# Optimization experiments

Measured on AMD Instinct MI355X. Metric: run time of the kernel, lower is better.

The kernel has to match this reference:

```python
import jax, jax.numpy as jnp
import numpy as np

N_ATOMS = 20000
N_CG = 1000
N_EDGES = 200000
FEAT = 128
N_RBF = 20
N_CONV = 3
CUTOFF = 5.0
EPS = 1e-15


def swish(x):
    return x * jax.nn.sigmoid(x)


def preprocess_r(r):
    # r: (n, 3) -> dist (n,), unit (n, 3)
    d = jnp.sqrt((r * r + EPS).sum(-1))
    return d, r / d[:, None]


def dist_embed(d, W, b):
    # PainnRadialBasis (learnable_k=False) + Dense + cosine envelope
    k = jnp.arange(1, N_RBF + 1, dtype=d.dtype)
    rbf = jnp.sin(k[None, :] * jnp.pi * d[:, None] / CUTOFF) / d[:, None]
    env = 0.5 * (jnp.cos(jnp.pi * d / CUTOFF) + 1.0) * (d < CUTOFF).astype(d.dtype)
    return (rbf @ W + b) * env[:, None]


def scatter_mean(x, idx, n):
    s = jax.ops.segment_sum(x, idx, num_segments=n)
    cnt = jax.ops.segment_sum(jnp.ones(idx.shape[0], x.dtype), idx, num_segments=n)
    cnt = jnp.maximum(cnt, 1.0)
    return s / cnt.reshape((n,) + (1,) * (x.ndim - 1))


def cg_encoder(z, xyz, cg_xyz, mapping, nbr_list, embed,
               msg_W1, msg_b1, msg_W2, msg_b2, msg_distW, msg_distb,
               upd_U, upd_V, upd_W1, upd_b1, upd_W2, upd_b2,
               cg_W1, cg_b1, cg_W2, cg_b2, cg_distW, cg_distb):
    s = embed[z]                                     # (N, F)
    v = jnp.zeros((s.shape[0], FEAT, 3), s.dtype)    # (N, F, 3)
    src, dst = nbr_list[:, 0], nbr_list[:, 1]
    r_ij = xyz[dst] - xyz[src]
    r_iI = xyz - cg_xyz[mapping]
    d_ij, u_ij = preprocess_r(r_ij)
    d_iI, u_iI = preprocess_r(r_iI)

    S_I = None
    V_I = None
    for i in range(N_CONV):
        # ---- MessageBlock ----
        phi = swish(s @ msg_W1[i] + msg_b1[i]) @ msg_W2[i] + msg_b2[i]          # (N, 3F)
        w_s = dist_embed(d_ij, msg_distW[i], msg_distb[i])                      # (E, 3F)
        inv = (phi[dst] * w_s).reshape(-1, 3, FEAT)                             # (E, 3, F)
        dv_ij = inv[:, 2, :, None] * u_ij[:, None, :] + inv[:, 0, :, None] * v[dst]
        s = s + jax.ops.segment_sum(inv[:, 1, :], src, num_segments=N_ATOMS)
        v = v + jax.ops.segment_sum(dv_ij, src, num_segments=N_ATOMS)
        # ---- UpdateBlock ----
        u_v = jnp.einsum('nfd,fg->ngd', v, upd_U[i])
        v_v = jnp.einsum('nfd,fg->ngd', v, upd_V[i])
        v_v_norm = jnp.sqrt((v_v * v_v + EPS).sum(-1))                          # (N, F)
        stack = swish(jnp.concatenate([s, v_v_norm], -1) @ upd_W1[i] + upd_b1[i]) @ upd_W2[i] + upd_b2[i]
        a_vv = stack[:, :FEAT, None]
        a_sv = stack[:, FEAT:2 * FEAT]
        a_ss = stack[:, 2 * FEAT:]
        v = v + u_v * a_vv
        s = s + (u_v * v_v).sum(-1) * a_sv + a_ss
        # ---- init CG features after first conv ----
        if i == 0:
            S_I = scatter_mean(s, mapping, N_CG)
            V_I = jnp.zeros((N_CG, FEAT, 3), s.dtype)
        # ---- ContractiveMessageBlock ----
        phi_cg = swish(s @ cg_W1[i] + cg_b1[i]) @ cg_W2[i] + cg_b2[i]           # (N, 3F)
        w_cg = dist_embed(d_iI, cg_distW[i], cg_distb[i])
        inv_cg = (phi_cg * w_cg).reshape(-1, 3, FEAT)
        dv_iI = inv_cg[:, 2, :, None] * u_iI[:, None, :] + inv_cg[:, 0, :, None] * v
        S_I = S_I + scatter_mean(inv_cg[:, 1, :], mapping, N_CG)
        V_I = V_I + scatter_mean(dv_iI, mapping, N_CG)
    return S_I


def setup_inputs() -> dict:
    key = jax.random.key(0)
    ks = jax.random.split(key, 20)
    p = lambda i, shape: jax.random.normal(ks[i], shape, jnp.float32) * 0.05
    return {
        'z': jax.random.randint(ks[0], (N_ATOMS,), 1, 100),
        'xyz': jax.random.normal(ks[1], (N_ATOMS, 3), jnp.float32),
        'cg_xyz': jax.random.normal(ks[2], (N_CG, 3), jnp.float32),
        'mapping': jax.random.randint(ks[3], (N_ATOMS,), 0, N_CG),
        'nbr_list': jax.random.randint(ks[4], (N_EDGES, 2), 0, N_ATOMS),
        'embed': p(5, (100, FEAT)).at[0].set(0.0),  # padding_idx=0
        'msg_W1': p(6, (N_CONV, FEAT, FEAT)), 'msg_b1': jnp.zeros((N_CONV, FEAT)),
        'msg_W2': p(7, (N_CONV, FEAT, 3 * FEAT)), 'msg_b2': jnp.zeros((N_CONV, 3 * FEAT)),
        'msg_distW': p(8, (N_CONV, N_RBF, 3 * FEAT)), 'msg_distb': jnp.zeros((N_CONV, 3 * FEAT)),
        'upd_U': p(9, (N_CONV, FEAT, FEAT)), 'upd_V': p(10, (N_CONV, FEAT, FEAT)),
        'upd_W1': p(11, (N_CONV, 2 * FEAT, FEAT)), 'upd_b1': jnp.zeros((N_CONV, FEAT)),
        'upd_W2': p(12, (N_CONV, FEAT, 3 * FEAT)), 'upd_b2': jnp.zeros((N_CONV, 3 * FEAT)),
        'cg_W1': p(13, (N_CONV, FEAT, FEAT)), 'cg_b1': jnp.zeros((N_CONV, FEAT)),
        'cg_W2': p(14, (N_CONV, FEAT, 3 * FEAT)), 'cg_b2': jnp.zeros((N_CONV, 3 * FEAT)),
        'cg_distW': p(15, (N_CONV, N_RBF, 3 * FEAT)), 'cg_distb': jnp.zeros((N_CONV, 3 * FEAT)),
    }


def reference(z, xyz, cg_xyz, mapping, nbr_list, embed,
              msg_W1, msg_b1, msg_W2, msg_b2, msg_distW, msg_distb,
              upd_U, upd_V, upd_W1, upd_b1, upd_W2, upd_b2,
              cg_W1, cg_b1, cg_W2, cg_b2, cg_distW, cg_distb):
    return cg_encoder(z, xyz, cg_xyz, mapping, nbr_list, embed,
                      msg_W1, msg_b1, msg_W2, msg_b2, msg_distW, msg_distb,
                      upd_U, upd_V, upd_W1, upd_b1, upd_W2, upd_b2,
                      cg_W1, cg_b1, cg_W2, cg_b2, cg_distW, cg_distb)
```

## Files before the change

### kernel.cpp

```cpp
#include <hip/hip_runtime.h>
#include <math.h>

#define N_ATOMS 20000
#define N_CG    1000
#define N_EDGES 200000
#define FEAT    128
#define NRBF    20
#define NCONV   3
#define CUTOFF  5.0f
#define PLANE   (N_ATOMS * FEAT)
#define PI_F    3.14159265358979323846f
#define LDH     130

#define PACK_PER_CONV 212992

typedef __attribute__((ext_vector_type(8))) short bf16x8;
typedef __attribute__((ext_vector_type(4))) float f32x4;

__device__ __forceinline__ void split2(float x, ushort& h, ushort& l)
{
    unsigned u  = __float_as_uint(x);
    unsigned hb = (u + 0x7FFFu + ((u >> 16) & 1u)) & 0xFFFF0000u;
    float    hf = __uint_as_float(hb);
    float    lf = x - hf;
    unsigned ul = __float_as_uint(lf);
    h = (ushort)(hb >> 16);
    l = (ushort)((ul + 0x7FFFu + ((ul >> 16) & 1u)) >> 16);
}

__device__ __forceinline__ float reconP(unsigned u)
{
    return __uint_as_float(u & 0xFFFF0000u) + __uint_as_float(u << 16);
}

__device__ __forceinline__ unsigned packP(float x)
{
    ushort h, l;
    split2(x, h, l);
    return ((unsigned)h << 16) | l;
}

__device__ __forceinline__ void splitv8(const float* hv, bf16x8& ah, bf16x8& al)
{
#pragma unroll
    for (int j = 0; j < 8; ++j) {
        ushort h, l;
        split2(hv[j], h, l);
        ah[j] = (short)h; al[j] = (short)l;
    }
}

__device__ __forceinline__ void unpack8(const unsigned* __restrict__ p,
                                        bf16x8& ah, bf16x8& al)
{
#pragma unroll
    for (int j = 0; j < 8; ++j) {
        unsigned u = p[j];
        ah[j] = (short)(u >> 16);
        al[j] = (short)(u & 0xFFFFu);
    }
}

#define MFMA3(ACC, AH_, AL_, BH_, BL_)                                              \
    ACC = __builtin_amdgcn_mfma_f32_16x16x32_bf16(AH_, BH_, ACC, 0, 0, 0);          \
    ACC = __builtin_amdgcn_mfma_f32_16x16x32_bf16(AH_, BL_, ACC, 0, 0, 0);          \
    ACC = __builtin_amdgcn_mfma_f32_16x16x32_bf16(AL_, BH_, ACC, 0, 0, 0);

template<int K1, int N2>
__global__ __launch_bounds__(256)
void mlp_fused(const ushort* __restrict__ AH, const ushort* __restrict__ AL,
               const ushort* __restrict__ B1h, const ushort* __restrict__ B1l,
               const float* __restrict__ b1,
               const ushort* __restrict__ B2h, const ushort* __restrict__ B2l,
               const float* __restrict__ b2, int bcol0,
               float* __restrict__ C)
{
    __shared__ float Hs[32 * LDH];
    const int tid  = threadIdx.x;
    const int lane = tid & 63;
    const int w    = tid >> 6;
    const int wm   = w & 1, wn = w >> 1;
    const int m0   = blockIdx.x * 32;
    const int l15  = lane & 15;
    const int koff = (lane >> 4) * 8;
    const int rowb = wm * 16;
    const int q4   = (lane >> 4) * 4;

    f32x4 acc1[4];
#pragma unroll
    for (int j = 0; j < 4; ++j) acc1[j] = (f32x4){0.f, 0.f, 0.f, 0.f};
#pragma unroll
    for (int k0 = 0; k0 < K1; k0 += 32) {
        size_t aa = (size_t)(m0 + rowb + l15) * K1 + k0 + koff;
        bf16x8 ah = *reinterpret_cast<const bf16x8*>(AH + aa);
        bf16x8 al = *reinterpret_cast<const bf16x8*>(AL + aa);
#pragma unroll
        for (int nf = 0; nf < 4; ++nf) {
            size_t ba = (size_t)(wn * 64 + nf * 16 + l15) * K1 + k0 + koff;
            bf16x8 bh = *reinterpret_cast<const bf16x8*>(B1h + ba);
            bf16x8 bl = *reinterpret_cast<const bf16x8*>(B1l + ba);
            MFMA3(acc1[nf], ah, al, bh, bl);
        }
    }
#pragma unroll
    for (int nf = 0; nf < 4; ++nf) {
        int col = wn * 64 + nf * 16 + l15;
        float bv = b1[col];
#pragma unroll
        for (int r = 0; r < 4; ++r) {
            float x = acc1[nf][r] + bv;
            x = x / (1.f + __expf(-x));
            Hs[(rowb + q4 + r) * LDH + col] = x;
        }
    }
    __syncthreads();

    constexpr int NF2  = N2 / 32;
    constexpr int WCOL = N2 / 2;
    f32x4 acc2[NF2];
#pragma unroll
    for (int j = 0; j < NF2; ++j) acc2[j] = (f32x4){0.f, 0.f, 0.f, 0.f};
#pragma unroll
    for (int k0 = 0; k0 < 128; k0 += 32) {
        const float* hp = &Hs[(rowb + l15) * LDH + k0 + koff];
        float hv[8];
#pragma unroll
        for (int j = 0; j < 8; ++j) hv[j] = hp[j];
        bf16x8 ah, al;
        splitv8(hv, ah, al);
#pragma unroll
        for (int nf = 0; nf < NF2; ++nf) {
            size_t ba = (size_t)(wn * WCOL + nf * 16 + l15) * 128 + k0 + koff;
            bf16x8 bh = *reinterpret_cast<const bf16x8*>(B2h + ba);
            bf16x8 bl = *reinterpret_cast<const bf16x8*>(B2l + ba);
            MFMA3(acc2[nf], ah, al, bh, bl);
        }
    }
#pragma unroll
    for (int nf = 0; nf < NF2; ++nf) {
        int col = wn * WCOL + nf * 16 + l15;
        float bv = b2 ? b2[bcol0 + col] : 0.f;
#pragma unroll
        for (int r = 0; r < 4; ++r) {
            int row = m0 + rowb + q4 + r;
            C[(size_t)row * N2 + col] = acc2[nf][r] + bv;
        }
    }
}

__global__ __launch_bounds__(256)
void mlp_dual(const ushort* __restrict__ AH, const ushort* __restrict__ AL,
              const ushort* __restrict__ B1mh, const ushort* __restrict__ B1ml,
              const float* __restrict__ b1m,
              const ushort* __restrict__ B2mh, const ushort* __restrict__ B2ml,
              const float* __restrict__ b2m,
              const ushort* __restrict__ B1ch, const ushort* __restrict__ B1cl,
              const float* __restrict__ b1c,
              const ushort* __restrict__ B2ch, const ushort* __restrict__ B2cl,
              const float* __restrict__ b2c,
              float* __restrict__ Cm, float* __restrict__ Cc)
{
    __shared__ float Hm[32 * LDH];
    __shared__ float Hc[32 * LDH];
    const int tid  = threadIdx.x;
    const int lane = tid & 63;
    const int w    = tid >> 6;
    const int wm   = w & 1, wn = w >> 1;
    const int m0   = blockIdx.x * 32;
    const int l15  = lane & 15;
    const int koff = (lane >> 4) * 8;
    const int rowb = wm * 16;
    const int q4   = (lane >> 4) * 4;

    f32x4 am[4], ac[4];
#pragma unroll
    for (int j = 0; j < 4; ++j) {
        am[j] = (f32x4){0.f, 0.f, 0.f, 0.f};
        ac[j] = (f32x4){0.f, 0.f, 0.f, 0.f};
    }
#pragma unroll
    for (int k0 = 0; k0 < 128; k0 += 32) {
        size_t aa = (size_t)(m0 + rowb + l15) * 128 + k0 + koff;
        bf16x8 ah = *reinterpret_cast<const bf16x8*>(AH + aa);
        bf16x8 al = *reinterpret_cast<const bf16x8*>(AL + aa);
#pragma unroll
        for (int nf = 0; nf < 4; ++nf) {
            size_t ba = (size_t)(wn * 64 + nf * 16 + l15) * 128 + k0 + koff;
            bf16x8 bmh = *reinterpret_cast<const bf16x8*>(B1mh + ba);
            bf16x8 bml = *reinterpret_cast<const bf16x8*>(B1ml + ba);
            MFMA3(am[nf], ah, al, bmh, bml);
            bf16x8 bch = *reinterpret_cast<const bf16x8*>(B1ch + ba);
            bf16x8 bcl = *reinterpret_cast<const bf16x8*>(B1cl + ba);
            MFMA3(ac[nf], ah, al, bch, bcl);
        }
    }
#pragma unroll
    for (int nf = 0; nf < 4; ++nf) {
        int col = wn * 64 + nf * 16 + l15;
        float bvm = b1m[col];
        float bvc = b1c[col];
#pragma unroll
        for (int r = 0; r < 4; ++r) {
            int lr = rowb + q4 + r;
            float x = am[nf][r] + bvm;
            Hm[lr * LDH + col] = x / (1.f + __expf(-x));
            float y = ac[nf][r] + bvc;
            Hc[lr * LDH + col] = y / (1.f + __expf(-y));
        }
    }
    __syncthreads();

    f32x4 a2m[12], a2c[4];
#pragma unroll
    for (int j = 0; j < 12; ++j) a2m[j] = (f32x4){0.f, 0.f, 0.f, 0.f};
#pragma unroll
    for (int j = 0; j < 4; ++j)  a2c[j] = (f32x4){0.f, 0.f, 0.f, 0.f};
#pragma unroll
    for (int k0 = 0; k0 < 128; k0 += 32) {
        const float* hpm = &Hm[(rowb + l15) * LDH + k0 + koff];
        const float* hpc = &Hc[(rowb + l15) * LDH + k0 + koff];
        float hvm[8], hvc[8];
#pragma unroll
        for (int j = 0; j < 8; ++j) { hvm[j] = hpm[j]; hvc[j] = hpc[j]; }
        bf16x8 ahm, alm, ahc, alc;
        splitv8(hvm, ahm, alm);
        splitv8(hvc, ahc, alc);
#pragma unroll
        for (int nf = 0; nf < 12; ++nf) {
            size_t ba = (size_t)(wn * 192 + nf * 16 + l15) * 128 + k0 + koff;
            bf16x8 bh = *reinterpret_cast<const bf16x8*>(B2mh + ba);
            bf16x8 bl = *reinterpret_cast<const bf16x8*>(B2ml + ba);
            MFMA3(a2m[nf], ahm, alm, bh, bl);
        }
#pragma unroll
        for (int nf = 0; nf < 4; ++nf) {
            size_t ba = (size_t)(wn * 64 + nf * 16 + l15) * 128 + k0 + koff;
            bf16x8 bh = *reinterpret_cast<const bf16x8*>(B2ch + ba);
            bf16x8 bl = *reinterpret_cast<const bf16x8*>(B2cl + ba);
            MFMA3(a2c[nf], ahc, alc, bh, bl);
        }
    }
#pragma unroll
    for (int nf = 0; nf < 12; ++nf) {
        int col = wn * 192 + nf * 16 + l15;
        float bv = b2m[col];
#pragma unroll
        for (int r = 0; r < 4; ++r) {
            int row = m0 + rowb + q4 + r;
            Cm[(size_t)row * 384 + col] = a2m[nf][r] + bv;
        }
    }
#pragma unroll
    for (int nf = 0; nf < 4; ++nf) {
        int col = wn * 64 + nf * 16 + l15;
        float bv = b2c[128 + col];
#pragma unroll
        for (int r = 0; r < 4; ++r) {
            int row = m0 + rowb + q4 + r;
            Cc[(size_t)row * 128 + col] = a2c[nf][r] + bv;
        }
    }
}

__global__ __launch_bounds__(256)
void k_update_mega(unsigned* __restrict__ vP,
                   const ushort* __restrict__ catH, const ushort* __restrict__ catL,
                   const ushort* __restrict__ BVh, const ushort* __restrict__ BVl,
                   const ushort* __restrict__ W1h, const ushort* __restrict__ W1l,
                   const float*  __restrict__ b1,
                   const ushort* __restrict__ W2h, const ushort* __restrict__ W2l,
                   const float*  __restrict__ b2,
                   const ushort* __restrict__ BUh, const ushort* __restrict__ BUl,
                   float* __restrict__ s,
                   ushort* __restrict__ sH, ushort* __restrict__ sL)
{
    __shared__ float  Hs[32 * LDH];
    __shared__ ushort nH[32 * 128];
    __shared__ ushort nL[32 * 128];

    const int tid  = threadIdx.x;
    const int lane = tid & 63;
    const int w    = tid >> 6;
    const int wm   = w & 1, wn = w >> 1;
    const int m0   = blockIdx.x * 32;
    const int l15  = lane & 15;
    const int koff = (lane >> 4) * 8;
    const int rowb = wm * 16;
    const int q4   = (lane >> 4) * 4;

    f32x4 accV[3][4], accU[3][4];
#pragma unroll
    for (int d = 0; d < 3; ++d)
#pragma unroll
        for (int j = 0; j < 4; ++j) {
            accV[d][j] = (f32x4){0.f, 0.f, 0.f, 0.f};
            accU[d][j] = (f32x4){0.f, 0.f, 0.f, 0.f};
        }
    for (int k0 = 0; k0 < 128; k0 += 32) {
        bf16x8 ah[3], al[3];
#pragma unroll
        for (int d = 0; d < 3; ++d) {
            size_t aa = (size_t)d * PLANE + (size_t)(m0 + rowb + l15) * 128 + k0 + koff;
            unsigned u[8];
#pragma unroll
            for (int j = 0; j < 8; ++j) u[j] = vP[aa + j];
            unpack8(u, ah[d], al[d]);
        }
#pragma unroll
        for (int nf = 0; nf < 4; ++nf) {
            size_t ba = (size_t)(wn * 64 + nf * 16 + l15) * 128 + k0 + koff;
            bf16x8 bvh = *reinterpret_cast<const bf16x8*>(BVh + ba);
            bf16x8 bvl = *reinterpret_cast<const bf16x8*>(BVl + ba);
            bf16x8 buh = *reinterpret_cast<const bf16x8*>(BUh + ba);
            bf16x8 bul = *reinterpret_cast<const bf16x8*>(BUl + ba);
#pragma unroll
            for (int d = 0; d < 3; ++d) {
                MFMA3(accV[d][nf], ah[d], al[d], bvh, bvl);
            }
#pragma unroll
            for (int d = 0; d < 3; ++d) {
                MFMA3(accU[d][nf], ah[d], al[d], buh, bul);
            }
        }
    }
#pragma unroll
    for (int nf = 0; nf < 4; ++nf) {
        int col = wn * 64 + nf * 16 + l15;
#pragma unroll
        for (int r = 0; r < 4; ++r) {
            int lrow = rowb + q4 + r;
            float x = accV[0][nf][r], y = accV[1][nf][r], z = accV[2][nf][r];
            float nrm = sqrtf(x * x + y * y + z * z + 3e-15f);
            ushort h, l;
            split2(nrm, h, l);
            nH[lrow * 128 + col] = h;
            nL[lrow * 128 + col] = l;
        }
    }
    __syncthreads();

    f32x4 acc1[4];
#pragma unroll
    for (int j = 0; j < 4; ++j) acc1[j] = (f32x4){0.f, 0.f, 0.f, 0.f};
#pragma unroll 2
    for (int k0 = 0; k0 < 256; k0 += 32) {
        bf16x8 ah, al;
        if (k0 < 128) {
            size_t aa = (size_t)(m0 + rowb + l15) * 128 + k0 + koff;
            ah = *reinterpret_cast<const bf16x8*>(catH + aa);
            al = *reinterpret_cast<const bf16x8*>(catL + aa);
        } else {
            int la = (rowb + l15) * 128 + (k0 - 128) + koff;
            ah = *reinterpret_cast<const bf16x8*>(nH + la);
            al = *reinterpret_cast<const bf16x8*>(nL + la);
        }
#pragma unroll
        for (int nf = 0; nf < 4; ++nf) {
            size_t ba = (size_t)(wn * 64 + nf * 16 + l15) * 256 + k0 + koff;
            bf16x8 bh = *reinterpret_cast<const bf16x8*>(W1h + ba);
            bf16x8 bl = *reinterpret_cast<const bf16x8*>(W1l + ba);
            MFMA3(acc1[nf], ah, al, bh, bl);
        }
    }
#pragma unroll
    for (int nf = 0; nf < 4; ++nf) {
        int col = wn * 64 + nf * 16 + l15;
        float bv = b1[col];
#pragma unroll
        for (int r = 0; r < 4; ++r) {
            float x = acc1[nf][r] + bv;
            x = x / (1.f + __expf(-x));
            Hs[(rowb + q4 + r) * LDH + col] = x;
        }
    }
    __syncthreads();

    f32x4 acc2[12];
#pragma unroll
    for (int j = 0; j < 12; ++j) acc2[j] = (f32x4){0.f, 0.f, 0.f, 0.f};
    for (int k0 = 0; k0 < 128; k0 += 32) {
        const float* hp = &Hs[(rowb + l15) * LDH + k0 + koff];
        float hv[8];
#pragma unroll
        for (int j = 0; j < 8; ++j) hv[j] = hp[j];
        bf16x8 ah, al;
        splitv8(hv, ah, al);
#pragma unroll
        for (int g = 0; g < 3; ++g) {
#pragma unroll
            for (int j = 0; j < 4; ++j) {
                size_t ba = (size_t)(g * 128 + wn * 64 + j * 16 + l15) * 128 + k0 + koff;
                bf16x8 bh = *reinterpret_cast<const bf16x8*>(W2h + ba);
                bf16x8 bl = *reinterpret_cast<const bf16x8*>(W2l + ba);
                MFMA3(acc2[g * 4 + j], ah, al, bh, bl);
            }
        }
    }

#pragma unroll
    for (int nf = 0; nf < 4; ++nf) {
        int col = wn * 64 + nf * 16 + l15;
        float bavv = b2[col];
        float basv = b2[128 + col];
        float bass = b2[256 + col];
#pragma unroll
        for (int r = 0; r < 4; ++r) {
            int row = m0 + rowb + q4 + r;
            size_t idx = (size_t)row * FEAT + col;
            float avv = acc2[nf][r]     + bavv;
            float asv = acc2[4 + nf][r] + basv;
            float ass = acc2[8 + nf][r] + bass;
            float u0 = accU[0][nf][r], u1 = accU[1][nf][r], u2 = accU[2][nf][r];
            float w0 = accV[0][nf][r], w1 = accV[1][nf][r], w2 = accV[2][nf][r];
            float dot = u0 * w0 + u1 * w1 + u2 * w2;
            float n0 = reconP(vP[idx])                      + u0 * avv;
            float n1 = reconP(vP[PLANE + idx])              + u1 * avv;
            float n2 = reconP(vP[2 * (size_t)PLANE + idx])  + u2 * avv;
            vP[idx] = packP(n0);
            vP[PLANE + idx] = packP(n1);
            vP[2 * (size_t)PLANE + idx] = packP(n2);
            float ns = s[idx] + dot * asv + ass;
            s[idx] = ns;
            ushort h, l;
            split2(ns, h, l); sH[idx] = h; sL[idx] = l;
        }
    }
}

__global__ void k_pack_all(const float* __restrict__ msg_W1, const float* __restrict__ msg_W2,
                           const float* __restrict__ upd_V,  const float* __restrict__ upd_W1,
                           const float* __restrict__ upd_W2, const float* __restrict__ upd_U,
                           const float* __restrict__ cg_W1,  const float* __restrict__ cg_W2,
                           ushort* __restrict__ Bh, ushort* __restrict__ Bl)
{
    const int wid = blockIdx.y, conv = blockIdx.z;
    const float* W; int K, N, ldw, col0; size_t off;
    switch (wid) {
        case 0: W = msg_W1 + (size_t)conv * 16384; K = 128; N = 128; ldw = 128; col0 = 0;   off = 0;      break;
        case 1: W = msg_W2 + (size_t)conv * 49152; K = 128; N = 384; ldw = 384; col0 = 0;   off = 16384;  break;
        case 2: W = upd_V  + (size_t)conv * 16384; K = 128; N = 128; ldw = 128; col0 = 0;   off = 65536;  break;
        case 3: W = upd_W1 + (size_t)conv * 32768; K = 256; N = 128; ldw = 128; col0 = 0;   off = 81920;  break;
        case 4: W = upd_W2 + (size_t)conv * 49152; K = 128; N = 384; ldw = 384; col0 = 0;   off = 114688; break;
        case 5: W = upd_U  + (size_t)conv * 16384; K = 128; N = 128; ldw = 128; col0 = 0;   off = 163840; break;
        case 6: W = cg_W1  + (size_t)conv * 16384; K = 128; N = 128; ldw = 128; col0 = 0;   off = 180224; break;
        default:W = cg_W2  + (size_t)conv * 49152; K = 128; N = 128; ldw = 384; col0 = 128; off = 196608; break;
    }
    off += (size_t)conv * PACK_PER_CONV;
    int idx = blockIdx.x * 256 + threadIdx.x;
    if (idx >= K * N) return;
    int k = idx & (K - 1);
    int n = idx >> ((K == 256) ? 8 : 7);
    ushort h, l;
    split2(W[(size_t)k * ldw + col0 + n], h, l);
    Bh[off + (size_t)n * K + k] = h;
    Bl[off + (size_t)n * K + k] = l;
}

__global__ void k_s_init(const int* __restrict__ z, const float* __restrict__ embed,
                         float* __restrict__ s, ushort* __restrict__ sH, ushort* __restrict__ sL)
{
    int idx = blockIdx.x * blockDim.x + threadIdx.x;
    if (idx >= PLANE) return;
    int n = idx >> 7, g = idx & 127;
    float e = embed[z[n] * FEAT + g];
    s[idx] = e;
    ushort h, l;
    split2(e, h, l);
    sH[idx] = h; sL[idx] = l;
}

__global__ void k_atom_geo(const int* __restrict__ mapping,
                           const float* __restrict__ xyz, const float* __restrict__ cg_xyz,
                           float* __restrict__ rbf_a, float* __restrict__ env_a,
                           float* __restrict__ cnt)
{
    int n = blockIdx.x * blockDim.x + threadIdx.x;
    if (n >= N_ATOMS) return;
    int m = mapping[n];
    float dx = xyz[n * 3 + 0] - cg_xyz[m * 3 + 0];
    float dy = xyz[n * 3 + 1] - cg_xyz[m * 3 + 1];
    float dz = xyz[n * 3 + 2] - cg_xyz[m * 3 + 2];
    float d = sqrtf(dx * dx + dy * dy + dz * dz + 3e-15f);
    float env = (d < CUTOFF) ? 0.5f * (cosf(PI_F * d / CUTOFF) + 1.f) : 0.f;
    env_a[n] = env;
    float s = env / d;
#pragma unroll
    for (int k = 0; k < NRBF; ++k)
        rbf_a[n * NRBF + k] = sinf((k + 1) * PI_F * d / CUTOFF) * s;
    atomicAdd(&cnt[m], 1.f);
}

__global__ void k_deg(const int* __restrict__ nbr, int* __restrict__ deg)
{
    int e = blockIdx.x * blockDim.x + threadIdx.x;
    if (e < N_EDGES) atomicAdd(&deg[nbr[2 * e]], 1);
}

__global__ __launch_bounds__(1024)
void k_scan(const int* __restrict__ deg, int* __restrict__ rowptr)
{
    __shared__ int sh[1024];
    const int chunk = (N_ATOMS + 1023) / 1024;
    int t = threadIdx.x;
    int base = t * chunk;
    int sum = 0;
    for (int i = 0; i < chunk; ++i) {
        int idx = base + i;
        if (idx < N_ATOMS) sum += deg[idx];
    }
    sh[t] = sum;
    __syncthreads();
    for (int off = 1; off < 1024; off <<= 1) {
        int val = (t >= off) ? sh[t - off] : 0;
        __syncthreads();
        sh[t] += val;
        __syncthreads();
    }
    int run = (t == 0) ? 0 : sh[t - 1];
    for (int i = 0; i < chunk; ++i) {
        int idx = base + i;
        if (idx < N_ATOMS) { rowptr[idx] = run; run += deg[idx]; }
    }
}

__global__ void k_fill(const int* __restrict__ nbr, const float* __restrict__ xyz,
                       const int* __restrict__ rowptr, int* __restrict__ cursor,
                       int* __restrict__ rec_dst, float4* __restrict__ rec_u4,
                       float* __restrict__ rec_rbf)
{
    int e = blockIdx.x * blockDim.x + threadIdx.x;
    if (e >= N_EDGES) return;
    int src = nbr[2 * e], dst = nbr[2 * e + 1];
    int pos = atomicAdd(&cursor[src], 1);
    int q = rowptr[src] + pos;
    float dx = xyz[dst * 3 + 0] - xyz[src * 3 + 0];
    float dy = xyz[dst * 3 + 1] - xyz[src * 3 + 1];
    float dz = xyz[dst * 3 + 2] - xyz[src * 3 + 2];
    float d = sqrtf(dx * dx + dy * dy + dz * dz + 3e-15f);
    float env = (d < CUTOFF) ? 0.5f * (cosf(PI_F * d / CUTOFF) + 1.f) : 0.f;
    rec_dst[q] = dst;
    rec_u4[q] = make_float4(dx / d, dy / d, dz / d, env);
    float sc = env / d;
#pragma unroll
    for (int k = 0; k < NRBF; ++k)
        rec_rbf[(size_t)q * NRBF + k] = sinf((k + 1) * PI_F * d / CUTOFF) * sc;
}

#define EDGE_BLOCKS 2500
__global__ __launch_bounds__(512, 2)
void k_edge_seg(const int* __restrict__ rowptr, const int* __restrict__ deg,
                const int* __restrict__ rec_dst, const float4* __restrict__ rec_u4,
                const float* __restrict__ rec_rbf,
                const float* __restrict__ phi,
                const unsigned* __restrict__ vPi, unsigned* __restrict__ vPo,
                float* __restrict__ s,
                ushort* __restrict__ catH, ushort* __restrict__ catL,
                const float* __restrict__ distW, const float* __restrict__ distb)
{
    const int tid    = threadIdx.x;
    const int slot   = tid >> 7;
    const int f      = tid & 127;
    const int slot_g = blockIdx.x * 4 + slot;
    const int nslots = EDGE_BLOCKS * 4;

    float wx[21], wy[21], wz[21];
#pragma unroll
    for (int k = 0; k < NRBF; ++k) {
        wx[k] = distW[k * 384 + f];
        wy[k] = distW[k * 384 + 128 + f];
        wz[k] = distW[k * 384 + 256 + f];
    }
    wx[20] = distb[f];
    wy[20] = distb[128 + f];
    wz[20] = distb[256 + f];
#pragma unroll
    for (int k = 0; k < 21; ++k) {
        asm volatile("" : "+v"(wx[k]), "+v"(wy[k]), "+v"(wz[k]));
    }

    for (int a = slot_g; a < N_ATOMS; a += nslots) {
        const int beg = rowptr[a];
        const int end = beg + deg[a];
        float s_acc = 0.f, vx = 0.f, vy = 0.f, vz = 0.f;

        for (int p = beg; p < end; p += 2) {
            const int  has2 = (p + 1 < end);
            const int  p1   = has2 ? p + 1 : p;
            const float m1  = has2 ? 1.f : 0.f;

            float4 u40 = rec_u4[p];
            float4 u41 = rec_u4[p1];
            int dst0 = rec_dst[p];
            int dst1 = rec_dst[p1];

            const float* ph0 = phi + (size_t)dst0 * 384 + f;
            const float* ph1 = phi + (size_t)dst1 * 384 + f;
            float p00 = ph0[0], p01 = ph0[128], p02 = ph0[256];
            float p10 = ph1[0], p11 = ph1[128], p12 = ph1[256];
            size_t di0 = (size_t)dst0 * FEAT + f;
            size_t di1 = (size_t)dst1 * FEAT + f;
            float v0x = reconP(vPi[di0]);
            float v0y = reconP(vPi[PLANE + di0]);
            float v0z = reconP(vPi[2 * (size_t)PLANE + di0]);
            float v1x = reconP(vPi[di1]);
            float v1y = reconP(vPi[PLANE + di1]);
            float v1z = reconP(vPi[2 * (size_t)PLANE + di1]);
            const float4* rb0 = reinterpret_cast<const float4*>(rec_rbf + (size_t)p  * NRBF);
            const float4* rb1 = reinterpret_cast<const float4*>(rec_rbf + (size_t)p1 * NRBF);
            float4 a0 = rb0[0], a1 = rb0[1], a2 = rb0[2], a3 = rb0[3], a4 = rb0[4];
            float4 b0 = rb1[0], b1 = rb1[1], b2 = rb1[2], b3 = rb1[3], b4 = rb1[4];

            const float rr0[21] = {a0.x, a0.y, a0.z, a0.w, a1.x, a1.y, a1.z, a1.w,
                                   a2.x, a2.y, a2.z, a2.w, a3.x, a3.y, a3.z, a3.w,
                                   a4.x, a4.y, a4.z, a4.w, u40.w};
            const float rr1[21] = {b0.x, b0.y, b0.z, b0.w, b1.x, b1.y, b1.z, b1.w,
                                   b2.x, b2.y, b2.z, b2.w, b3.x, b3.y, b3.z, b3.w,
                                   b4.x, b4.y, b4.z, b4.w, u41.w};
            float w00 = 0.f, w01 = 0.f, w02 = 0.f;
            float w10 = 0.f, w11 = 0.f, w12 = 0.f;
#pragma unroll
            for (int k = 0; k < 21; ++k) {
                w00 += rr0[k] * wx[k];
                w01 += rr0[k] * wy[k];
                w02 += rr0[k] * wz[k];
                w10 += rr1[k] * wx[k];
                w11 += rr1[k] * wy[k];
                w12 += rr1[k] * wz[k];
            }
            float i00 = p00 * w00, i01 = p01 * w01, i02 = p02 * w02;
            float i10 = (p10 * w10) * m1, i11 = (p11 * w11) * m1, i12 = (p12 * w12) * m1;
            vx += i02 * u40.x + i00 * v0x;
            vy += i02 * u40.y + i00 * v0y;
            vz += i02 * u40.z + i00 * v0z;
            s_acc += i01;
            vx += i12 * u41.x + i10 * v1x;
            vy += i12 * u41.y + i10 * v1y;
            vz += i12 * u41.z + i10 * v1z;
            s_acc += i11;
        }

        size_t si = (size_t)a * FEAT + f;
        float ns = s[si] + s_acc;
        s[si] = ns;
        float nx = reconP(vPi[si])                     + vx;
        float ny = reconP(vPi[PLANE + si])             + vy;
        float nz = reconP(vPi[2 * (size_t)PLANE + si]) + vz;
        vPo[si] = packP(nx);
        vPo[PLANE + si] = packP(ny);
        vPo[2 * (size_t)PLANE + si] = packP(nz);
        ushort h, l;
        split2(ns, h, l);
        catH[(size_t)a * 128 + f] = h;
        catL[(size_t)a * 128 + f] = l;
    }
}

__global__ __launch_bounds__(128)
void k_cg_msg(const int* __restrict__ mapping, const float* __restrict__ phi_mid,
              const float* __restrict__ rbf_a, const float* __restrict__ env_a,
              const float* __restrict__ distW, const float* __restrict__ distb,
              const float* __restrict__ s_add, float* __restrict__ S_acc)
{
    int n = blockIdx.x;
    float env = env_a[n];
    int f = threadIdx.x;
    if (env == 0.f && s_add == nullptr) return;
    float val = s_add ? s_add[n * FEAT + f] : 0.f;
    if (env != 0.f) {
        __shared__ float sh_rbf[NRBF];
        if (f < NRBF) sh_rbf[f] = rbf_a[n * NRBF + f];
        __syncthreads();
        float w1 = 0.f;
#pragma unroll
        for (int k = 0; k < NRBF; ++k)
            w1 += sh_rbf[k] * distW[k * 384 + 128 + f];
        w1 += distb[128 + f] * env;
        val += phi_mid[n * FEAT + f] * w1;
    }
    atomicAdd(&S_acc[mapping[n] * FEAT + f], val);
}

__global__ void k_finalize(const float* __restrict__ S_acc, const float* __restrict__ cnt,
                           float* __restrict__ out, int add)
{
    int idx = blockIdx.x * blockDim.x + threadIdx.x;
    if (idx >= N_CG * FEAT) return;
    float val = S_acc[idx] / fmaxf(cnt[idx >> 7], 1.f);
    if (add) out[idx] += val;
    else     out[idx] = val;
}

extern "C" void kernel_launch(void* const* d_in, const int* in_sizes, int n_in,
                              void* d_out, int out_size, void* d_ws, size_t ws_size,
                              hipStream_t stream)
{
    const int*   z        = (const int*)d_in[0];
    const float* xyz      = (const float*)d_in[1];
    const float* cg_xyz   = (const float*)d_in[2];
    const int*   mapping  = (const int*)d_in[3];
    const int*   nbr      = (const int*)d_in[4];
    const float* embed    = (const float*)d_in[5];
    const float* msg_W1   = (const float*)d_in[6];
    const float* msg_b1   = (const float*)d_in[7];
    const float* msg_W2   = (const float*)d_in[8];
    const float* msg_b2   = (const float*)d_in[9];
    const float* msg_dW   = (const float*)d_in[10];
    const float* msg_db   = (const float*)d_in[11];
    const float* upd_U    = (const float*)d_in[12];
    const float* upd_V    = (const float*)d_in[13];
    const float* upd_W1   = (const float*)d_in[14];
    const float* upd_b1   = (const float*)d_in[15];
    const float* upd_W2   = (const float*)d_in[16];
    const float* upd_b2   = (const float*)d_in[17];
    const float* cg_W1    = (const float*)d_in[18];
    const float* cg_b1    = (const float*)d_in[19];
    const float* cg_W2    = (const float*)d_in[20];
    const float* cg_b2    = (const float*)d_in[21];
    const float* cg_dW    = (const float*)d_in[22];
    const float* cg_db    = (const float*)d_in[23];
    float* out = (float*)d_out;

    float* ws = (float*)d_ws;
    size_t o = 0;
    float* s      = ws + o; o += PLANE;
    float* uv     = ws + o; o += PLANE;
    float* phi    = ws + o; o += (size_t)N_ATOMS * 384;
    float* catpk  = ws + o; o += PLANE;
    float* spk    = ws + o; o += PLANE;
    unsigned* vPA = (unsigned*)(ws + o); o += 3 * PLANE;
    unsigned* vPB = (unsigned*)(ws + o); o += 3 * PLANE;
    float4* rec_u4 = (float4*)(ws + o); o += (size_t)N_EDGES * 4;
    float* rec_rbf = ws + o; o += (size_t)N_EDGES * NRBF;
    int*   rec_dst = (int*)(ws + o); o += N_EDGES;
    float* rbf_a  = ws + o; o += (size_t)N_ATOMS * NRBF;
    float* env_a  = ws + o; o += N_ATOMS;
    float* cnt    = ws + o; o += N_CG;
    float* S_acc  = ws + o; o += N_CG * FEAT;
    int*   deg    = (int*)(ws + o); o += N_ATOMS;
    int*   rowptr = (int*)(ws + o); o += N_ATOMS;
    int*   cursor = (int*)(ws + o); o += N_ATOMS;
    ushort* packH = (ushort*)(ws + o); o += (size_t)NCONV * PACK_PER_CONV / 2;
    ushort* packL = (ushort*)(ws + o); o += (size_t)NCONV * PACK_PER_CONV / 2;

    ushort* catH = (ushort*)catpk; ushort* catL = catH + (size_t)N_ATOMS * 128;
    ushort* sH = (ushort*)spk;  ushort* sL = sH + PLANE;

    hipMemsetAsync(vPA, 0, sizeof(unsigned) * 3 * PLANE, stream);
    hipMemsetAsync(cnt, 0, sizeof(float) * N_CG, stream);
    hipMemsetAsync(deg, 0, sizeof(int) * N_ATOMS, stream);
    hipMemsetAsync(cursor, 0, sizeof(int) * N_ATOMS, stream);
    k_pack_all<<<dim3(192, 8, 3), 256, 0, stream>>>(msg_W1, msg_W2, upd_V, upd_W1,
                                                    upd_W2, upd_U, cg_W1, cg_W2,
                                                    packH, packL);
    k_s_init<<<(PLANE + 255) / 256, 256, 0, stream>>>(z, embed, s, sH, sL);
    k_atom_geo<<<(N_ATOMS + 255) / 256, 256, 0, stream>>>(mapping, xyz, cg_xyz,
                                                          rbf_a, env_a, cnt);
    k_deg<<<(N_EDGES + 255) / 256, 256, 0, stream>>>(nbr, deg);
    k_scan<<<1, 1024, 0, stream>>>(deg, rowptr);
    k_fill<<<(N_EDGES + 255) / 256, 256, 0, stream>>>(nbr, xyz, rowptr, cursor,
                                                      rec_dst, rec_u4, rec_rbf);

    unsigned* vPc = vPA;
    unsigned* vPn = vPB;

    mlp_fused<128, 384><<<625, 256, 0, stream>>>(
        sH, sL, packH + 0, packL + 0, msg_b1,
        packH + 16384, packL + 16384, msg_b2, 0, phi);

    for (int i = 0; i < NCONV; ++i) {
        const float* ub1 = upd_b1 + (size_t)i * FEAT;
        const float* ub2 = upd_b2 + (size_t)i * 384;
        const float* mdW = msg_dW + (size_t)i * NRBF * 384;
        const float* mdb = msg_db + (size_t)i * 384;
        const float* cb1 = cg_b1  + (size_t)i * FEAT;
        const float* cb2 = cg_b2  + (size_t)i * 384;
        const float* cdW = cg_dW  + (size_t)i * NRBF * 384;
        const float* cdb = cg_db  + (size_t)i * 384;
        const size_t pb  = (size_t)i * PACK_PER_CONV;

        k_edge_seg<<<EDGE_BLOCKS, 512, 0, stream>>>(rowptr, deg, rec_dst, rec_u4,
                                                    rec_rbf, phi, vPc, vPn, s,
                                                    catH, catL, mdW, mdb);

        k_update_mega<<<625, 256, 0, stream>>>(
            vPn, catH, catL,
            packH + pb + 65536,  packL + pb + 65536,
            packH + pb + 81920,  packL + pb + 81920,
            ub1,
            packH + pb + 114688, packL + pb + 114688,
            ub2,
            packH + pb + 163840, packL + pb + 163840,
            s, sH, sL);

        if (i < NCONV - 1) {
            const size_t pn = (size_t)(i + 1) * PACK_PER_CONV;
            mlp_dual<<<625, 256, 0, stream>>>(
                sH, sL,
                packH + pn + 0,      packL + pn + 0,      msg_b1 + (size_t)(i + 1) * FEAT,
                packH + pn + 16384,  packL + pn + 16384,  msg_b2 + (size_t)(i + 1) * 384,
                packH + pb + 180224, packL + pb + 180224, cb1,
                packH + pb + 196608, packL + pb + 196608, cb2,
                phi, uv);
        } else {
            mlp_fused<128, 128><<<625, 256, 0, stream>>>(
                sH, sL, packH + pb + 180224, packL + pb + 180224, cb1,
                packH + pb + 196608, packL + pb + 196608, cb2, 128, uv);
        }

        hipMemsetAsync(S_acc, 0, sizeof(float) * N_CG * FEAT, stream);
        k_cg_msg<<<N_ATOMS, 128, 0, stream>>>(mapping, uv, rbf_a, env_a, cdW, cdb,
                                              (i == 0) ? s : nullptr, S_acc);
        k_finalize<<<(N_CG * FEAT + 255) / 256, 256, 0, stream>>>(S_acc, cnt, out,
                                                                  i == 0 ? 0 : 1);

        unsigned* t = vPn; vPn = vPc; vPc = t;
    }
}
```

Before: 1.301 ms.

## Fuse next-layer message and CG MLPs into update kernel epilogue

Folds the per-atom message MLP for the next convolution and the CG MLP into the end of the update kernel. The freshly split s tiles stay in shared memory and feed those GEMMs directly, instead of being written to global memory and read back by a separate launch. The per-iteration S_acc memset becomes one up-front memset over a separate buffer per convolution. This removes a launch and a global round-trip of s, at the cost of more shared memory and register pressure in the update kernel, which may lower occupancy.

```diff
diff --git a/kernel.cpp b/kernel.cpp
--- a/kernel.cpp
+++ b/kernel.cpp
@@ -148,120 +148,7 @@
     }
 }
 
-__global__ __launch_bounds__(256)
-void mlp_dual(const ushort* __restrict__ AH, const ushort* __restrict__ AL,
-              const ushort* __restrict__ B1mh, const ushort* __restrict__ B1ml,
-              const float* __restrict__ b1m,
-              const ushort* __restrict__ B2mh, const ushort* __restrict__ B2ml,
-              const float* __restrict__ b2m,
-              const ushort* __restrict__ B1ch, const ushort* __restrict__ B1cl,
-              const float* __restrict__ b1c,
-              const ushort* __restrict__ B2ch, const ushort* __restrict__ B2cl,
-              const float* __restrict__ b2c,
-              float* __restrict__ Cm, float* __restrict__ Cc)
-{
-    __shared__ float Hm[32 * LDH];
-    __shared__ float Hc[32 * LDH];
-    const int tid  = threadIdx.x;
-    const int lane = tid & 63;
-    const int w    = tid >> 6;
-    const int wm   = w & 1, wn = w >> 1;
-    const int m0   = blockIdx.x * 32;
-    const int l15  = lane & 15;
-    const int koff = (lane >> 4) * 8;
-    const int rowb = wm * 16;
-    const int q4   = (lane >> 4) * 4;
-
-    f32x4 am[4], ac[4];
-#pragma unroll
-    for (int j = 0; j < 4; ++j) {
-        am[j] = (f32x4){0.f, 0.f, 0.f, 0.f};
-        ac[j] = (f32x4){0.f, 0.f, 0.f, 0.f};
-    }
-#pragma unroll
-    for (int k0 = 0; k0 < 128; k0 += 32) {
-        size_t aa = (size_t)(m0 + rowb + l15) * 128 + k0 + koff;
-        bf16x8 ah = *reinterpret_cast<const bf16x8*>(AH + aa);
-        bf16x8 al = *reinterpret_cast<const bf16x8*>(AL + aa);
-#pragma unroll
-        for (int nf = 0; nf < 4; ++nf) {
-            size_t ba = (size_t)(wn * 64 + nf * 16 + l15) * 128 + k0 + koff;
-            bf16x8 bmh = *reinterpret_cast<const bf16x8*>(B1mh + ba);
-            bf16x8 bml = *reinterpret_cast<const bf16x8*>(B1ml + ba);
-            MFMA3(am[nf], ah, al, bmh, bml);
-            bf16x8 bch = *reinterpret_cast<const bf16x8*>(B1ch + ba);
-            bf16x8 bcl = *reinterpret_cast<const bf16x8*>(B1cl + ba);
-            MFMA3(ac[nf], ah, al, bch, bcl);
-        }
-    }
-#pragma unroll
-    for (int nf = 0; nf < 4; ++nf) {
-        int col = wn * 64 + nf * 16 + l15;
-        float bvm = b1m[col];
-        float bvc = b1c[col];
-#pragma unroll
-        for (int r = 0; r < 4; ++r) {
-            int lr = rowb + q4 + r;
-            float x = am[nf][r] + bvm;
-            Hm[lr * LDH + col] = x / (1.f + __expf(-x));
-            float y = ac[nf][r] + bvc;
-            Hc[lr * LDH + col] = y / (1.f + __expf(-y));
-        }
-    }
-    __syncthreads();
-
-    f32x4 a2m[12], a2c[4];
-#pragma unroll
-    for (int j = 0; j < 12; ++j) a2m[j] = (f32x4){0.f, 0.f, 0.f, 0.f};
-#pragma unroll
-    for (int j = 0; j < 4; ++j)  a2c[j] = (f32x4){0.f, 0.f, 0.f, 0.f};
-#pragma unroll
-    for (int k0 = 0; k0 < 128; k0 += 32) {
-        const float* hpm = &Hm[(rowb + l15) * LDH + k0 + koff];
-        const float* hpc = &Hc[(rowb + l15) * LDH + k0 + koff];
-        float hvm[8], hvc[8];
-#pragma unroll
-        for (int j = 0; j < 8; ++j) { hvm[j] = hpm[j]; hvc[j] = hpc[j]; }
-        bf16x8 ahm, alm, ahc, alc;
-        splitv8(hvm, ahm, alm);
-        splitv8(hvc, ahc, alc);
-#pragma unroll
-        for (int nf = 0; nf < 12; ++nf) {
-            size_t ba = (size_t)(wn * 192 + nf * 16 + l15) * 128 + k0 + koff;
-            bf16x8 bh = *reinterpret_cast<const bf16x8*>(B2mh + ba);
-            bf16x8 bl = *reinterpret_cast<const bf16x8*>(B2ml + ba);
-            MFMA3(a2m[nf], ahm, alm, bh, bl);
-        }
-#pragma unroll
-        for (int nf = 0; nf < 4; ++nf) {
-            size_t ba = (size_t)(wn * 64 + nf * 16 + l15) * 128 + k0 + koff;
-            bf16x8 bh = *reinterpret_cast<const bf16x8*>(B2ch + ba);
-            bf16x8 bl = *reinterpret_cast<const bf16x8*>(B2cl + ba);
-            MFMA3(a2c[nf], ahc, alc, bh, bl);
-        }
-    }
-#pragma unroll
-    for (int nf = 0; nf < 12; ++nf) {
-        int col = wn * 192 + nf * 16 + l15;
-        float bv = b2m[col];
-#pragma unroll
-        for (int r = 0; r < 4; ++r) {
-            int row = m0 + rowb + q4 + r;
-            Cm[(size_t)row * 384 + col] = a2m[nf][r] + bv;
-        }
-    }
-#pragma unroll
-    for (int nf = 0; nf < 4; ++nf) {
-        int col = wn * 64 + nf * 16 + l15;
-        float bv = b2c[128 + col];
-#pragma unroll
-        for (int r = 0; r < 4; ++r) {
-            int row = m0 + rowb + q4 + r;
-            Cc[(size_t)row * 128 + col] = a2c[nf][r] + bv;
-        }
-    }
-}
-
+template<int HAS_MSG>
 __global__ __launch_bounds__(256)
 void k_update_mega(unsigned* __restrict__ vP,
                    const ushort* __restrict__ catH, const ushort* __restrict__ catL,
@@ -272,11 +159,23 @@
                    const float*  __restrict__ b2,
                    const ushort* __restrict__ BUh, const ushort* __restrict__ BUl,
                    float* __restrict__ s,
-                   ushort* __restrict__ sH, ushort* __restrict__ sL)
-{
-    __shared__ float  Hs[32 * LDH];
-    __shared__ ushort nH[32 * 128];
-    __shared__ ushort nL[32 * 128];
+                   const ushort* __restrict__ M1h, const ushort* __restrict__ M1l,
+                   const float*  __restrict__ m1b,
+                   const ushort* __restrict__ M2h, const ushort* __restrict__ M2l,
+                   const float*  __restrict__ m2b,
+                   const ushort* __restrict__ C1h, const ushort* __restrict__ C1l,
+                   const float*  __restrict__ c1b,
+                   const ushort* __restrict__ C2h, const ushort* __restrict__ C2l,
+                   const float*  __restrict__ c2b,
+                   float* __restrict__ phi, float* __restrict__ uv)
+{
+    __shared__ __align__(16) char smem[16640 + 16384 + 16640];
+    float*  Hs  = (float*)smem;
+    ushort* nH  = (ushort*)(smem + 16640);
+    ushort* nL  = (ushort*)(smem + 16640 + 8192);
+    ushort* sHs = nH;
+    ushort* sLs = nL;
+    float*  Hc  = (float*)(smem + 16640 + 16384);
 
     const int tid  = threadIdx.x;
     const int lane = tid & 63;
@@ -405,7 +304,8 @@
         float bass = b2[256 + col];
 #pragma unroll
         for (int r = 0; r < 4; ++r) {
-            int row = m0 + rowb + q4 + r;
+            int lrow = rowb + q4 + r;
+            int row  = m0 + lrow;
             size_t idx = (size_t)row * FEAT + col;
             float avv = acc2[nf][r]     + bavv;
             float asv = acc2[4 + nf][r] + basv;
@@ -422,7 +322,113 @@
             float ns = s[idx] + dot * asv + ass;
             s[idx] = ns;
             ushort h, l;
-            split2(ns, h, l); sH[idx] = h; sL[idx] = l;
+            split2(ns, h, l);
+            sHs[lrow * 128 + col] = h;
+            sLs[lrow * 128 + col] = l;
+        }
+    }
+    __syncthreads();
+
+    f32x4 am[4], ac[4];
+#pragma unroll
+    for (int j = 0; j < 4; ++j) {
+        am[j] = (f32x4){0.f, 0.f, 0.f, 0.f};
+        ac[j] = (f32x4){0.f, 0.f, 0.f, 0.f};
+    }
+#pragma unroll
+    for (int k0 = 0; k0 < 128; k0 += 32) {
+        int la = (rowb + l15) * 128 + k0 + koff;
+        bf16x8 ah = *reinterpret_cast<const bf16x8*>(sHs + la);
+        bf16x8 al = *reinterpret_cast<const bf16x8*>(sLs + la);
+#pragma unroll
+        for (int nf = 0; nf < 4; ++nf) {
+            size_t ba = (size_t)(wn * 64 + nf * 16 + l15) * 128 + k0 + koff;
+            if (HAS_MSG) {
+                bf16x8 bh = *reinterpret_cast<const bf16x8*>(M1h + ba);
+                bf16x8 bl = *reinterpret_cast<const bf16x8*>(M1l + ba);
+                MFMA3(am[nf], ah, al, bh, bl);
+            }
+            bf16x8 ch = *reinterpret_cast<const bf16x8*>(C1h + ba);
+            bf16x8 cl = *reinterpret_cast<const bf16x8*>(C1l + ba);
+            MFMA3(ac[nf], ah, al, ch, cl);
+        }
+    }
+#pragma unroll
+    for (int nf = 0; nf < 4; ++nf) {
+        int col = wn * 64 + nf * 16 + l15;
+        float bvc = c1b[col];
+        float bvm = HAS_MSG ? m1b[col] : 0.f;
+#pragma unroll
+        for (int r = 0; r < 4; ++r) {
+            int lr = rowb + q4 + r;
+            if (HAS_MSG) {
+                float x = am[nf][r] + bvm;
+                Hs[lr * LDH + col] = x / (1.f + __expf(-x));
+            }
+            float y = ac[nf][r] + bvc;
+            Hc[lr * LDH + col] = y / (1.f + __expf(-y));
+        }
+    }
+    __syncthreads();
+
+    f32x4 a2m[12], a2c[4];
+    if (HAS_MSG) {
+#pragma unroll
+        for (int j = 0; j < 12; ++j) a2m[j] = (f32x4){0.f, 0.f, 0.f, 0.f};
+    }
+#pragma unroll
+    for (int j = 0; j < 4; ++j)  a2c[j] = (f32x4){0.f, 0.f, 0.f, 0.f};
+#pragma unroll
+    for (int k0 = 0; k0 < 128; k0 += 32) {
+        const float* hpc = &Hc[(rowb + l15) * LDH + k0 + koff];
+        float hvc[8];
+#pragma unroll
+        for (int j = 0; j < 8; ++j) hvc[j] = hpc[j];
+        bf16x8 ahc, alc;
+        splitv8(hvc, ahc, alc);
+#pragma unroll
+        for (int nf = 0; nf < 4; ++nf) {
+            size_t ba = (size_t)(wn * 64 + nf * 16 + l15) * 128 + k0 + koff;
+            bf16x8 bh = *reinterpret_cast<const bf16x8*>(C2h + ba);
+            bf16x8 bl = *reinterpret_cast<const bf16x8*>(C2l + ba);
+            MFMA3(a2c[nf], ahc, alc, bh, bl);
+        }
+        if (HAS_MSG) {
+            const float* hpm = &Hs[(rowb + l15) * LDH + k0 + koff];
+            float hvm[8];
+#pragma unroll
+            for (int j = 0; j < 8; ++j) hvm[j] = hpm[j];
+            bf16x8 ahm, alm;
+            splitv8(hvm, ahm, alm);
+#pragma unroll
+            for (int nf = 0; nf < 12; ++nf) {
+                size_t ba = (size_t)(wn * 192 + nf * 16 + l15) * 128 + k0 + koff;
+                bf16x8 bh = *reinterpret_cast<const bf16x8*>(M2h + ba);
+                bf16x8 bl = *reinterpret_cast<const bf16x8*>(M2l + ba);
+                MFMA3(a2m[nf], ahm, alm, bh, bl);
+            }
+        }
+    }
+    if (HAS_MSG) {
+#pragma unroll
+        for (int nf = 0; nf < 12; ++nf) {
+            int col = wn * 192 + nf * 16 + l15;
+            float bv = m2b[col];
+#pragma unroll
+            for (int r = 0; r < 4; ++r) {
+                int row = m0 + rowb + q4 + r;
+                phi[(size_t)row * 384 + col] = a2m[nf][r] + bv;
+            }
+        }
+    }
+#pragma unroll
+    for (int nf = 0; nf < 4; ++nf) {
+        int col = wn * 64 + nf * 16 + l15;
+        float bv = c2b[128 + col];
+#pragma unroll
+        for (int r = 0; r < 4; ++r) {
+            int row = m0 + rowb + q4 + r;
+            uv[(size_t)row * 128 + col] = a2c[nf][r] + bv;
         }
     }
 }
@@ -735,7 +741,7 @@
     float* rbf_a  = ws + o; o += (size_t)N_ATOMS * NRBF;
     float* env_a  = ws + o; o += N_ATOMS;
     float* cnt    = ws + o; o += N_CG;
-    float* S_acc  = ws + o; o += N_CG * FEAT;
+    float* S_acc  = ws + o; o += (size_t)NCONV * N_CG * FEAT;
     int*   deg    = (int*)(ws + o); o += N_ATOMS;
     int*   rowptr = (int*)(ws + o); o += N_ATOMS;
     int*   cursor = (int*)(ws + o); o += N_ATOMS;
@@ -749,6 +755,7 @@
     hipMemsetAsync(cnt, 0, sizeof(float) * N_CG, stream);
     hipMemsetAsync(deg, 0, sizeof(int) * N_ATOMS, stream);
     hipMemsetAsync(cursor, 0, sizeof(int) * N_ATOMS, stream);
+    hipMemsetAsync(S_acc, 0, sizeof(float) * NCONV * N_CG * FEAT, stream);
     k_pack_all<<<dim3(192, 8, 3), 256, 0, stream>>>(msg_W1, msg_W2, upd_V, upd_W1,
                                                     upd_W2, upd_U, cg_W1, cg_W2,
                                                     packH, packL);
@@ -777,40 +784,49 @@
         const float* cdW = cg_dW  + (size_t)i * NRBF * 384;
         const float* cdb = cg_db  + (size_t)i * 384;
         const size_t pb  = (size_t)i * PACK_PER_CONV;
+        float* Sa = S_acc + (size_t)i * N_CG * FEAT;
 
         k_edge_seg<<<EDGE_BLOCKS, 512, 0, stream>>>(rowptr, deg, rec_dst, rec_u4,
                                                     rec_rbf, phi, vPc, vPn, s,
                                                     catH, catL, mdW, mdb);
 
-        k_update_mega<<<625, 256, 0, stream>>>(
-            vPn, catH, catL,
-            packH + pb + 65536,  packL + pb + 65536,
-            packH + pb + 81920,  packL + pb + 81920,
-            ub1,
-            packH + pb + 114688, packL + pb + 114688,
-            ub2,
-            packH + pb + 163840, packL + pb + 163840,
-            s, sH, sL);
-
         if (i < NCONV - 1) {
             const size_t pn = (size_t)(i + 1) * PACK_PER_CONV;
-            mlp_dual<<<625, 256, 0, stream>>>(
-                sH, sL,
-                packH + pn + 0,      packL + pn + 0,      msg_b1 + (size_t)(i + 1) * FEAT,
-                packH + pn + 16384,  packL + pn + 16384,  msg_b2 + (size_t)(i + 1) * 384,
+            k_update_mega<1><<<625, 256, 0, stream>>>(
+                vPn, catH, catL,
+                packH + pb + 65536,  packL + pb + 65536,
+                packH + pb + 81920,  packL + pb + 81920,
+                ub1,
+                packH + pb + 114688, packL + pb + 114688,
+                ub2,
+                packH + pb + 163840, packL + pb + 163840,
+                s,
+                packH + pn + 0,      packL + pn + 0,
+                msg_b1 + (size_t)(i + 1) * FEAT,
+                packH + pn + 16384,  packL + pn + 16384,
+                msg_b2 + (size_t)(i + 1) * 384,
                 packH + pb + 180224, packL + pb + 180224, cb1,
                 packH + pb + 196608, packL + pb + 196608, cb2,
                 phi, uv);
         } else {
-            mlp_fused<128, 128><<<625, 256, 0, stream>>>(
-                sH, sL, packH + pb + 180224, packL + pb + 180224, cb1,
-                packH + pb + 196608, packL + pb + 196608, cb2, 128, uv);
-        }
-
-        hipMemsetAsync(S_acc, 0, sizeof(float) * N_CG * FEAT, stream);
+            k_update_mega<0><<<625, 256, 0, stream>>>(
+                vPn, catH, catL,
+                packH + pb + 65536,  packL + pb + 65536,
+                packH + pb + 81920,  packL + pb + 81920,
+                ub1,
+                packH + pb + 114688, packL + pb + 114688,
+                ub2,
+                packH + pb + 163840, packL + pb + 163840,
+                s,
+                nullptr, nullptr, nullptr, nullptr, nullptr, nullptr,
+                packH + pb + 180224, packL + pb + 180224, cb1,
+                packH + pb + 196608, packL + pb + 196608, cb2,
+                phi, uv);
+        }
+
         k_cg_msg<<<N_ATOMS, 128, 0, stream>>>(mapping, uv, rbf_a, env_a, cdW, cdb,
-                                              (i == 0) ? s : nullptr, S_acc);
-        k_finalize<<<(N_CG * FEAT + 255) / 256, 256, 0, stream>>>(S_acc, cnt, out,
+                                              (i == 0) ? s : nullptr, Sa);
+        k_finalize<<<(N_CG * FEAT + 255) / 256, 256, 0, stream>>>(Sa, cnt, out,
                                                                   i == 0 ? 0 : 1);
 
         unsigned* t = vPn; vPn = vPc; vPc = t;
```

Result: no change. 1.313 ms (+1.0%).
